# Performance work log

Hardware: AMD Instinct MI355X
Metric: run time of the kernel (lower is better)

## Reference

```python
import jax, jax.numpy as jnp
import numpy as np

TEMPERATURE = 0.5


def setup_inputs() -> dict:
    key = jax.random.key(0)
    k1, k2 = jax.random.split(key)
    B, C, H, W = 64, 256, 32, 32
    inputs = jax.random.normal(k1, (B, C, H, W), dtype=jnp.float32)
    targets = jax.random.normal(k2, (B, C, H, W), dtype=jnp.float32)
    return {"inputs": inputs, "targets": targets}


def reference(inputs, targets):
    # [B, C, H, W] -> [H, W, B, C]
    x = jnp.transpose(inputs, (2, 3, 0, 1))
    y = jnp.transpose(targets, (2, 3, 0, 1))
    B = x.shape[-2]
    feats = jnp.concatenate([x, y], axis=-2)  # [H, W, 2B, C]
    eps = jnp.finfo(feats.dtype).eps
    # cosine similarity: normalize each vector with eps-clamped norm, then dot
    norms = jnp.maximum(jnp.linalg.norm(feats, axis=-1, keepdims=True), eps)
    fn = feats / norms
    sim = jnp.einsum('hwic,hwjc->hwij', fn, fn)  # [H, W, 2B, 2B]
    # mask self-similarity diagonal with -inf
    mask = jnp.eye(2 * B, dtype=bool)
    sim = jnp.where(mask, -jnp.inf, sim)
    log_sm = jax.nn.log_softmax(sim / TEMPERATURE, axis=-1)
    pos = jnp.concatenate(
        [jnp.diagonal(log_sm, offset=B, axis1=-2, axis2=-1),
         jnp.diagonal(log_sm, offset=-B, axis1=-2, axis2=-1)],
        axis=-1,
    )  # [H, W, 2B]
    return -jnp.mean(pos)
```

## Files before the change

### kernel.cpp

```cpp
#include <hip/hip_runtime.h>
#include <stdint.h>

#define HWPOS 1024
#define CCH   256
#define RROWS 128
#define EPSF  1.1920928955078125e-07f

typedef __attribute__((ext_vector_type(8))) short   short8;
typedef __attribute__((ext_vector_type(4))) float   float4v;

__device__ __forceinline__ unsigned short f2bf(float f) {
  uint32_t x = __float_as_uint(f);
  x += 0x7FFFu + ((x >> 16) & 1u);
  return (unsigned short)(x >> 16);
}

__global__ __launch_bounds__(256) void k_transpose(const float* __restrict__ inp,
                                                   const float* __restrict__ tgt,
                                                   unsigned short* __restrict__ wsF) {
  __shared__ float lbuf[256 * 36];
  const int t   = threadIdx.x;
  const int r   = blockIdx.y;
  const int hw0 = blockIdx.x * 32;
  const float* src = (r < 64) ? (inp + (size_t)r * CCH * HWPOS)
                              : (tgt + (size_t)(r - 64) * CCH * HWPOS);
  {
    const int hq = t & 7;
    const int cc = t >> 3;
#pragma unroll
    for (int ci = 0; ci < 8; ++ci) {
      int c = ci * 32 + cc;
      float4 g = *(const float4*)(src + (size_t)c * HWPOS + hw0 + hq * 4);
      *(float4*)&lbuf[c * 36 + hq * 4] = g;
    }
  }
  __syncthreads();
  const int m  = r & 7;
  const int j  = t & 7;
  const int h  = t >> 3;
#pragma unroll
  for (int g = 0; g < 4; ++g) {
    int slot = g * 8 + j;
    int c8   = g * 8 + (j ^ m);
    float v[8];
#pragma unroll
    for (int e = 0; e < 8; ++e) v[e] = lbuf[(c8 * 8 + e) * 36 + h];
    uint4 o;
    o.x = f2bf(v[0]) | ((uint32_t)f2bf(v[1]) << 16);
    o.y = f2bf(v[2]) | ((uint32_t)f2bf(v[3]) << 16);
    o.z = f2bf(v[4]) | ((uint32_t)f2bf(v[5]) << 16);
    o.w = f2bf(v[6]) | ((uint32_t)f2bf(v[7]) << 16);
    size_t base = ((size_t)(hw0 + h) * RROWS + r) * CCH + slot * 8;
    *(uint4*)(wsF + base) = o;
  }
}

__global__ __launch_bounds__(512, 4) void k_gram(const unsigned short* __restrict__ wsF,
                                                 float* __restrict__ partials) {
  __shared__ unsigned short Fs[RROWS * CCH];
  __shared__ float sInv[RROWS];
  __shared__ float wred[8];
  const int t  = threadIdx.x;
  const int hw = blockIdx.x;
  {
    const int4* g4 = (const int4*)(wsF + (size_t)hw * (RROWS * CCH));
    int4* l4 = (int4*)Fs;
#pragma unroll
    for (int it = 0; it < 8; ++it) l4[it * 512 + t] = g4[it * 512 + t];
  }
  __syncthreads();
  const int lane = t & 63;
  const int w    = t >> 6;
  const int lid  = lane & 15;
  const int quad = lane >> 4;
  const int lm   = lid & 7;
  float4v acc[8];
#pragma unroll
  for (int ni = 0; ni < 8; ++ni) acc[ni] = (float4v){0.f, 0.f, 0.f, 0.f};
  const int baseA = ((w << 4) | lid) * CCH;
#pragma unroll
  for (int ks = 0; ks < 8; ++ks) {
    const int off = (((ks * 4 + quad) ^ lm) << 3);
    short8 a = *(const short8*)&Fs[baseA + off];
#pragma unroll
    for (int ni = 0; ni < 8; ++ni) {
      short8 b = *(const short8*)&Fs[((ni << 4) | lid) * CCH + off];
      acc[ni] = __builtin_amdgcn_mfma_f32_16x16x32_bf16(a, b, acc[ni], 0, 0, 0);
    }
  }
  if ((lid >> 2) == quad) {
    float nrm = fmaxf(sqrtf(acc[w][lid & 3]), EPSF);
    sInv[(w << 4) | lid] = 1.0f / nrm;
  }
  __syncthreads();
  float invj[8];
#pragma unroll
  for (int ni = 0; ni < 8; ++ni) invj[ni] = sInv[(ni << 4) | lid];
  float lacc = 0.f;
#pragma unroll
  for (int reg = 0; reg < 4; ++reg) {
    const int rloc = quad * 4 + reg;
    const int rg   = (w << 4) | rloc;
    const float invi = sInv[rg];
    float v[8];
#pragma unroll
    for (int ni = 0; ni < 8; ++ni) v[ni] = 2.0f * acc[ni][reg] * invi * invj[ni];
    if (lid == rloc) v[w] = -3.0e38f;
    float mx = v[0];
#pragma unroll
    for (int ni = 1; ni < 8; ++ni) mx = fmaxf(mx, v[ni]);
#pragma unroll
    for (int s = 1; s < 16; s <<= 1) mx = fmaxf(mx, __shfl_xor(mx, s, 16));
    float sm = 0.f;
#pragma unroll
    for (int ni = 0; ni < 8; ++ni) sm += expf(v[ni] - mx);
#pragma unroll
    for (int s = 1; s < 16; s <<= 1) sm += __shfl_xor(sm, s, 16);
    const float lse = mx + logf(sm);
    const int jp = (rg + 64) & 127;
    const float cand = v[jp >> 4];
    const float vp = __shfl(cand, jp & 15, 16);
    lacc += vp - lse;
  }
#pragma unroll
  for (int s = 1; s < 64; s <<= 1) lacc += __shfl_xor(lacc, s, 64);
  if (lane == 0) wred[w] = lacc;
  __syncthreads();
  if (t == 0) {
    float tot = 0.f;
#pragma unroll
    for (int i = 0; i < 8; ++i) tot += wred[i];
    partials[hw] = tot;
  }
}

__global__ __launch_bounds__(256) void k_reduce(const float* __restrict__ partials,
                                                float* __restrict__ out) {
  __shared__ float wr[4];
  const int t = threadIdx.x;
  float s = 0.f;
#pragma unroll
  for (int i = 0; i < 4; ++i) s += partials[t + i * 256];
#pragma unroll
  for (int sh = 1; sh < 64; sh <<= 1) s += __shfl_xor(s, sh, 64);
  if ((t & 63) == 0) wr[t >> 6] = s;
  __syncthreads();
  if (t == 0) {
    out[0] = -(wr[0] + wr[1] + wr[2] + wr[3]) / (131072.0f * 16.0f);
  }
}

extern "C" void kernel_launch(void* const* d_in, const int* in_sizes, int n_in,
                              void* d_out, int out_size, void* d_ws, size_t ws_size,
                              hipStream_t stream) {
  const float* inp = (const float*)d_in[0];
  const float* tgt = (const float*)d_in[1];
  unsigned short* wsF = (unsigned short*)d_ws;
  float* partials = (float*)((char*)d_ws + (size_t)HWPOS * RROWS * CCH * 2);
  k_transpose<<<dim3(32, 128), 256, 0, stream>>>(inp, tgt, wsF);
  k_gram<<<dim3(HWPOS), 512, 0, stream>>>(wsF, partials);
  k_reduce<<<1, 256, 0, stream>>>(partials, (float*)d_out);
}
```

Measured before the change: 188.4 us.

## Drop LDS staging in transpose, use direct global-to-LDS loads, fast exp/log

```diff
diff --git a/kernel.cpp b/kernel.cpp
--- a/kernel.cpp
+++ b/kernel.cpp
@@ -18,41 +18,34 @@
 __global__ __launch_bounds__(256) void k_transpose(const float* __restrict__ inp,
                                                    const float* __restrict__ tgt,
                                                    unsigned short* __restrict__ wsF) {
-  __shared__ float lbuf[256 * 36];
   const int t   = threadIdx.x;
+  const int j   = t & 7;
+  const int h   = (t >> 3) & 7;
+  const int g   = t >> 6;
   const int r   = blockIdx.y;
-  const int hw0 = blockIdx.x * 32;
+  const int hw0 = blockIdx.x * 16;
+  const int m   = r & 7;
+  const int slot = g * 8 + j;
+  const int c8   = g * 8 + (j ^ m);
   const float* src = (r < 64) ? (inp + (size_t)r * CCH * HWPOS)
                               : (tgt + (size_t)(r - 64) * CCH * HWPOS);
-  {
-    const int hq = t & 7;
-    const int cc = t >> 3;
+  const float* p = src + (size_t)c8 * 8 * HWPOS + hw0 + h * 2;
+  float2 v[8];
 #pragma unroll
-    for (int ci = 0; ci < 8; ++ci) {
-      int c = ci * 32 + cc;
-      float4 g = *(const float4*)(src + (size_t)c * HWPOS + hw0 + hq * 4);
-      *(float4*)&lbuf[c * 36 + hq * 4] = g;
-    }
-  }
-  __syncthreads();
-  const int m  = r & 7;
-  const int j  = t & 7;
-  const int h  = t >> 3;
-#pragma unroll
-  for (int g = 0; g < 4; ++g) {
-    int slot = g * 8 + j;
-    int c8   = g * 8 + (j ^ m);
-    float v[8];
-#pragma unroll
-    for (int e = 0; e < 8; ++e) v[e] = lbuf[(c8 * 8 + e) * 36 + h];
-    uint4 o;
-    o.x = f2bf(v[0]) | ((uint32_t)f2bf(v[1]) << 16);
-    o.y = f2bf(v[2]) | ((uint32_t)f2bf(v[3]) << 16);
-    o.z = f2bf(v[4]) | ((uint32_t)f2bf(v[5]) << 16);
-    o.w = f2bf(v[6]) | ((uint32_t)f2bf(v[7]) << 16);
-    size_t base = ((size_t)(hw0 + h) * RROWS + r) * CCH + slot * 8;
-    *(uint4*)(wsF + base) = o;
-  }
+  for (int e = 0; e < 8; ++e) v[e] = *(const float2*)(p + (size_t)e * HWPOS);
+  uint4 oa, ob;
+  oa.x = f2bf(v[0].x) | ((uint32_t)f2bf(v[1].x) << 16);
+  oa.y = f2bf(v[2].x) | ((uint32_t)f2bf(v[3].x) << 16);
+  oa.z = f2bf(v[4].x) | ((uint32_t)f2bf(v[5].x) << 16);
+  oa.w = f2bf(v[6].x) | ((uint32_t)f2bf(v[7].x) << 16);
+  ob.x = f2bf(v[0].y) | ((uint32_t)f2bf(v[1].y) << 16);
+  ob.y = f2bf(v[2].y) | ((uint32_t)f2bf(v[3].y) << 16);
+  ob.z = f2bf(v[4].y) | ((uint32_t)f2bf(v[5].y) << 16);
+  ob.w = f2bf(v[6].y) | ((uint32_t)f2bf(v[7].y) << 16);
+  const size_t ba = ((size_t)(hw0 + h * 2)     * RROWS + r) * CCH + slot * 8;
+  const size_t bb = ((size_t)(hw0 + h * 2 + 1) * RROWS + r) * CCH + slot * 8;
+  *(uint4*)(wsF + ba) = oa;
+  *(uint4*)(wsF + bb) = ob;
 }
 
 __global__ __launch_bounds__(512, 4) void k_gram(const unsigned short* __restrict__ wsF,
@@ -63,10 +56,14 @@
   const int t  = threadIdx.x;
   const int hw = blockIdx.x;
   {
-    const int4* g4 = (const int4*)(wsF + (size_t)hw * (RROWS * CCH));
-    int4* l4 = (int4*)Fs;
+    const unsigned short* gsrc = wsF + (size_t)hw * (RROWS * CCH);
 #pragma unroll
-    for (int it = 0; it < 8; ++it) l4[it * 512 + t] = g4[it * 512 + t];
+    for (int it = 0; it < 8; ++it) {
+      __builtin_amdgcn_global_load_lds(
+          (const __attribute__((address_space(1))) unsigned int*)(gsrc + (size_t)(it * 512 + t) * 8),
+          (__attribute__((address_space(3))) unsigned int*)(Fs + (size_t)(it * 512 + t) * 8),
+          16, 0, 0);
+    }
   }
   __syncthreads();
   const int lane = t & 63;
@@ -113,10 +110,10 @@
     for (int s = 1; s < 16; s <<= 1) mx = fmaxf(mx, __shfl_xor(mx, s, 16));
     float sm = 0.f;
 #pragma unroll
-    for (int ni = 0; ni < 8; ++ni) sm += expf(v[ni] - mx);
+    for (int ni = 0; ni < 8; ++ni) sm += __expf(v[ni] - mx);
 #pragma unroll
     for (int s = 1; s < 16; s <<= 1) sm += __shfl_xor(sm, s, 16);
-    const float lse = mx + logf(sm);
+    const float lse = mx + __logf(sm);
     const int jp = (rg + 64) & 127;
     const float cand = v[jp >> 4];
     const float vp = __shfl(cand, jp & 15, 16);
@@ -157,7 +154,7 @@
   const float* tgt = (const float*)d_in[1];
   unsigned short* wsF = (unsigned short*)d_ws;
   float* partials = (float*)((char*)d_ws + (size_t)HWPOS * RROWS * CCH * 2);
-  k_transpose<<<dim3(32, 128), 256, 0, stream>>>(inp, tgt, wsF);
+  k_transpose<<<dim3(64, 128), 256, 0, stream>>>(inp, tgt, wsF);
   k_gram<<<dim3(HWPOS), 512, 0, stream>>>(wsF, partials);
   k_reduce<<<1, 256, 0, stream>>>(partials, (float*)d_out);
 }
```

Result: slower. 197.2 us (+4.7%).
